# Kernel optimization log

Hardware: AMD Instinct MI355X
Metric: run time of the kernel (lower is better)

## Reference

```python
import jax, jax.numpy as jnp
import numpy as np

COL_IDX = 5  # colIdx: column used as sort key
REVERSE = False


def setup_inputs() -> dict:
    key = jax.random.key(0)
    # x: [batch, seq, feat]
    x = jax.random.normal(key, (32, 4096, 256), dtype=jnp.float32)
    return {"x": x}


def reference(x):
    # tf.nn.top_k(x[:, :, nc], k=S) returns indices of a full descending sort
    # with stable tie-breaking (earlier index first). jnp.argsort is stable,
    # so argsort of the negated key reproduces it exactly.
    keys = x[:, :, COL_IDX]                       # [B, S]
    idxs = jnp.argsort(-keys, axis=1)             # [B, S] descending order
    if REVERSE:
        idxs = idxs[:, ::-1]
    # gather_nd with (batch, idx) pairs == take_along_axis over the seq dim
    return jnp.take_along_axis(x, idxs[:, :, None], axis=1)  # [B, S, F]
```

## Files before the change

kernel.cpp:

```cpp
#include <hip/hip_runtime.h>
#include <stdint.h>

#define BATCH   32
#define ROWS    4096
#define COLS    256
#define COL_IDX 5

typedef unsigned long long u64;
typedef unsigned int       u32;

__global__ __launch_bounds__(256)
void extract_keys_kernel(const float* __restrict__ x, u64* __restrict__ keys) {
    const int i = blockIdx.x * 256 + threadIdx.x;
    u32 u = __float_as_uint(x[(size_t)i * COLS + COL_IDX]);
    u = (u >> 31) ? ~u : (u | 0x80000000u);
    u = ~u;
    keys[i] = ((u64)u << 32) | (u32)(i & (ROWS - 1));
}

__global__ __launch_bounds__(256, 4)
void rank_copy_kernel(const float* __restrict__ x,
                      const u64* __restrict__ keys,
                      float* __restrict__ out) {
    __shared__ int part[4][64];
    const int w    = (int)threadIdx.x >> 6;
    const int lane = (int)threadIdx.x & 63;
    const int b    = blockIdx.x >> 6;
    const int r0   = (blockIdx.x & 63) << 6;
    const u64* __restrict__ kb = keys + (size_t)b * ROWS;

    const int jbeg = w * (ROWS / 4);
    u64 kv[16];
    #pragma unroll
    for (int t = 0; t < 16; ++t)
        kv[t] = kb[jbeg + t * 64 + lane];

    const u64 my    = kb[r0 + lane];
    const u32 my_lo = (u32)my, my_hi = (u32)(my >> 32);

    int vrank = 0;
    #pragma unroll 2
    for (int m = 0; m < 64; ++m) {
        const u32 klo = (u32)__builtin_amdgcn_readlane((int)my_lo, m);
        const u32 khi = (u32)__builtin_amdgcn_readlane((int)my_hi, m);
        const u64 mym = ((u64)khi << 32) | klo;
        int rank_m = 0;
        #pragma unroll
        for (int t = 0; t < 16; ++t)
            rank_m += (int)__popcll(__ballot(kv[t] < mym));
        vrank = (lane == m) ? rank_m : vrank;
    }

    part[w][lane] = vrank;
    __syncthreads();
    const int total = part[0][lane] + part[1][lane]
                    + part[2][lane] + part[3][lane];

    const float4* __restrict__ src  =
        (const float4*)(x + ((size_t)b * ROWS + r0) * COLS);
    float4* __restrict__ outb = (float4*)(out + (size_t)b * ROWS * COLS);
    #pragma unroll 4
    for (int t = 0; t < 16; ++t) {
        const int l   = w * 16 + t;
        const int dst = __builtin_amdgcn_readlane(total, l);
        outb[(size_t)dst * 64 + lane] = src[(size_t)l * 64 + lane];
    }
}

extern "C" void kernel_launch(void* const* d_in, const int* in_sizes, int n_in,
                              void* d_out, int out_size, void* d_ws, size_t ws_size,
                              hipStream_t stream) {
    const float* x   = (const float*)d_in[0];
    float*       out = (float*)d_out;
    u64*         keys = (u64*)d_ws;

    extract_keys_kernel<<<(BATCH * ROWS) / 256, 256, 0, stream>>>(x, keys);
    rank_copy_kernel<<<BATCH * 64, 256, 0, stream>>>(x, keys, out);
}
```

Before: 243.2 us.

## Split fused rank+copy kernel into separate rank and scatter-copy kernels

```diff
diff --git a/kernel.cpp b/kernel.cpp
--- a/kernel.cpp
+++ b/kernel.cpp
@@ -18,10 +18,8 @@
     keys[i] = ((u64)u << 32) | (u32)(i & (ROWS - 1));
 }
 
-__global__ __launch_bounds__(256, 4)
-void rank_copy_kernel(const float* __restrict__ x,
-                      const u64* __restrict__ keys,
-                      float* __restrict__ out) {
+__global__ __launch_bounds__(256)
+void rank_kernel(const u64* __restrict__ keys, u32* __restrict__ dstg) {
     __shared__ int part[4][64];
     const int w    = (int)threadIdx.x >> 6;
     const int lane = (int)threadIdx.x & 63;
@@ -34,10 +32,9 @@
     #pragma unroll
     for (int t = 0; t < 16; ++t)
         kv[t] = kb[jbeg + t * 64 + lane];
+    const u64 my = kb[r0 + lane];
 
-    const u64 my    = kb[r0 + lane];
     const u32 my_lo = (u32)my, my_hi = (u32)(my >> 32);
-
     int vrank = 0;
     #pragma unroll 2
     for (int m = 0; m < 64; ++m) {
@@ -53,17 +50,27 @@
 
     part[w][lane] = vrank;
     __syncthreads();
-    const int total = part[0][lane] + part[1][lane]
-                    + part[2][lane] + part[3][lane];
+    if (w == 0) {
+        const int total = part[0][lane] + part[1][lane]
+                        + part[2][lane] + part[3][lane];
+        dstg[(size_t)b * ROWS + r0 + lane] = (u32)(b * ROWS) + (u32)total;
+    }
+}
 
-    const float4* __restrict__ src  =
-        (const float4*)(x + ((size_t)b * ROWS + r0) * COLS);
-    float4* __restrict__ outb = (float4*)(out + (size_t)b * ROWS * COLS);
-    #pragma unroll 4
-    for (int t = 0; t < 16; ++t) {
-        const int l   = w * 16 + t;
-        const int dst = __builtin_amdgcn_readlane(total, l);
-        outb[(size_t)dst * 64 + lane] = src[(size_t)l * 64 + lane];
+__global__ __launch_bounds__(256)
+void scatter_copy_kernel(const float* __restrict__ x,
+                         const u32* __restrict__ dstg,
+                         float* __restrict__ out) {
+    const int w    = (int)threadIdx.x >> 6;
+    const int lane = (int)threadIdx.x & 63;
+    const int rg0  = blockIdx.x * 16 + w * 4;
+    const float4* __restrict__ src = (const float4*)x;
+    float4* __restrict__ o = (float4*)out;
+    #pragma unroll
+    for (int t = 0; t < 4; ++t) {
+        const int rg  = rg0 + t;
+        const u32 dg  = dstg[rg];
+        o[(size_t)dg * 64 + lane] = src[(size_t)rg * 64 + lane];
     }
 }
 
@@ -73,7 +80,9 @@
     const float* x   = (const float*)d_in[0];
     float*       out = (float*)d_out;
     u64*         keys = (u64*)d_ws;
+    u32*         dstg = (u32*)((char*)d_ws + (size_t)BATCH * ROWS * 8);
 
     extract_keys_kernel<<<(BATCH * ROWS) / 256, 256, 0, stream>>>(x, keys);
-    rank_copy_kernel<<<BATCH * 64, 256, 0, stream>>>(x, keys, out);
+    rank_kernel<<<BATCH * 64, 256, 0, stream>>>(keys, dstg);
+    scatter_copy_kernel<<<(BATCH * ROWS) / 16, 256, 0, stream>>>(x, dstg, out);
 }
```

Measured after the change: 270.3 us. +11.1%, slower.
